# Optimization experiments

Measured on AMD Instinct MI355X. Metric: run time of the kernel, lower is better.

The kernel has to match this reference:

```python
import jax, jax.numpy as jnp
import numpy as np

N_USERS = 1_000_000
N_ITEMS = 100_000
LATENT = 64
BATCH = 4096


def setup_inputs() -> dict:
    key = jax.random.key(0)
    k1, k2, k3, k4 = jax.random.split(key, 4)
    # Xavier-normal init: std = sqrt(2 / (fan_in + fan_out))
    uw_std = float(np.sqrt(2.0 / (N_USERS + LATENT)))
    iw_std = float(np.sqrt(2.0 / (N_ITEMS + LATENT)))
    return {
        "user_ids": jax.random.randint(k1, (BATCH,), 0, N_USERS, dtype=jnp.int32),
        "item_ids": jax.random.randint(k2, (BATCH,), 0, N_ITEMS, dtype=jnp.int32),
        "user_weight": jax.random.normal(k3, (N_USERS, LATENT), dtype=jnp.float32) * uw_std,
        "item_weight": jax.random.normal(k4, (N_ITEMS, LATENT), dtype=jnp.float32) * iw_std,
        "user_bias": jnp.zeros((N_USERS, 1), dtype=jnp.float32),
        "item_bias": jnp.zeros((N_ITEMS, 1), dtype=jnp.float32),
        "bias": jnp.zeros((1,), dtype=jnp.float32),
    }


def reference(user_ids, item_ids, user_weight, item_weight, user_bias, item_bias, bias):
    # Gather rows for the requested users/items.
    uw = user_weight[user_ids]          # [Bu, d]
    ub = user_bias[user_ids]            # [Bu, 1]
    iw = item_weight[item_ids]          # [Bi, d]
    ib = item_bias[item_ids]            # [Bi, 1]
    # rating[u, i] = <uw_u, iw_i> + ub_u + ib_i + bias
    rating = jnp.einsum("ud,id->ui", uw, iw) + ub + ib.T + bias
    # pass_through_sigmoid=False, so no sigmoid applied.
    return rating
```

## Files before the change

### kernel.cpp

```cpp
#include <hip/hip_runtime.h>


#define BATCH 4096
#define D     64
#define TILE  64

__global__ __launch_bounds__(256) void pmf_tile_kernel(
    const int*   __restrict__ user_ids,
    const int*   __restrict__ item_ids,
    const float* __restrict__ user_weight,
    const float* __restrict__ item_weight,
    const float* __restrict__ user_bias,
    const float* __restrict__ item_bias,
    const float* __restrict__ bias,
    float*       __restrict__ out)
{
    __shared__ float Ut[D][TILE];
    __shared__ float It[D][TILE];
    __shared__ float ubs[TILE];
    __shared__ float ibs[TILE];

    const int t  = threadIdx.x;
    const int bx = blockIdx.x;
    const int by = blockIdx.y;

    const int r = t >> 2;
    const int q = t & 3;
    const int urow = user_ids[by * TILE + r];
    const int irow = item_ids[bx * TILE + r];
    const float* up = user_weight + (size_t)urow * D;
    const float* ip = item_weight + (size_t)irow * D;
    #pragma unroll
    for (int i = 0; i < 4; ++i) {
        const int k0 = q * 4 + i * 16;
        const float4 uv = *(const float4*)(up + k0);
        const float4 iv = *(const float4*)(ip + k0);
        Ut[k0 + 0][r] = uv.x; Ut[k0 + 1][r] = uv.y;
        Ut[k0 + 2][r] = uv.z; Ut[k0 + 3][r] = uv.w;
        It[k0 + 0][r] = iv.x; It[k0 + 1][r] = iv.y;
        It[k0 + 2][r] = iv.z; It[k0 + 3][r] = iv.w;
    }
    if (t < TILE) {
        ubs[t] = user_bias[user_ids[by * TILE + t]];
    } else if (t < 2 * TILE) {
        const int tt = t - TILE;
        ibs[tt] = item_bias[item_ids[bx * TILE + tt]];
    }
    __syncthreads();

    const int tx = t & 15;
    const int ty = t >> 4;

    float acc[4][4] = {{0.f}};
    #pragma unroll 16
    for (int k = 0; k < D; ++k) {
        const float4 u  = *(const float4*)&Ut[k][ty * 4];
        const float4 iv = *(const float4*)&It[k][tx * 4];
        const float uu[4] = {u.x, u.y, u.z, u.w};
        const float ii[4] = {iv.x, iv.y, iv.z, iv.w};
        #pragma unroll
        for (int a = 0; a < 4; ++a)
            #pragma unroll
            for (int b = 0; b < 4; ++b)
                acc[a][b] = fmaf(uu[a], ii[b], acc[a][b]);
    }

    const float gb = bias[0];
    #pragma unroll
    for (int a = 0; a < 4; ++a) {
        const int row = by * TILE + ty * 4 + a;
        const float ub = ubs[ty * 4 + a] + gb;
        float4 o;
        o.x = acc[a][0] + ub + ibs[tx * 4 + 0];
        o.y = acc[a][1] + ub + ibs[tx * 4 + 1];
        o.z = acc[a][2] + ub + ibs[tx * 4 + 2];
        o.w = acc[a][3] + ub + ibs[tx * 4 + 3];
        *(float4*)(out + (size_t)row * BATCH + bx * TILE + tx * 4) = o;
    }
}

extern "C" void kernel_launch(void* const* d_in, const int* in_sizes, int n_in,
                              void* d_out, int out_size, void* d_ws, size_t ws_size,
                              hipStream_t stream) {
    const int*   user_ids    = (const int*)  d_in[0];
    const int*   item_ids    = (const int*)  d_in[1];
    const float* user_weight = (const float*)d_in[2];
    const float* item_weight = (const float*)d_in[3];
    const float* user_bias   = (const float*)d_in[4];
    const float* item_bias   = (const float*)d_in[5];
    const float* bias        = (const float*)d_in[6];
    float* out = (float*)d_out;

    dim3 grid(BATCH / TILE, BATCH / TILE);
    dim3 block(256);
    pmf_tile_kernel<<<grid, block, 0, stream>>>(
        user_ids, item_ids, user_weight, item_weight,
        user_bias, item_bias, bias, out);
}
```

Before: 349.7 us.

## Use bf16 MFMA with 128x128 tiles for the gathered rating outer product

Gathered user and item rows are converted to bf16 in shared memory and the dot products run on 16x16x32 bf16 MFMA instructions instead of scalar FP32 FMAs. Tiles grow from 64x64 to 128x128 with four waves each covering 64x64, and shared rows are padded to reduce bank conflicts. This targets compute throughput, but the kernel writes a 64 MB output and is likely store-bound. The output stores are now scalar and strided per lane rather than float4, and bf16 inputs reduce dot-product precision.

```diff
diff --git a/kernel.cpp b/kernel.cpp
--- a/kernel.cpp
+++ b/kernel.cpp
@@ -3,9 +3,20 @@
 
 #define BATCH 4096
 #define D     64
-#define TILE  64
+#define BM    128
+#define BN    128
+#define ROWSZ 72
 
-__global__ __launch_bounds__(256) void pmf_tile_kernel(
+typedef __attribute__((ext_vector_type(8))) short bf16x8;
+typedef __attribute__((ext_vector_type(4))) float f32x4;
+
+static __device__ __forceinline__ unsigned short f2bf(float x) {
+    unsigned int u = __builtin_bit_cast(unsigned int, x);
+    u += 0x7FFFu + ((u >> 16) & 1u);
+    return (unsigned short)(u >> 16);
+}
+
+__global__ __launch_bounds__(256) void pmf_mfma_kernel(
     const int*   __restrict__ user_ids,
     const int*   __restrict__ item_ids,
     const float* __restrict__ user_weight,
@@ -15,67 +26,88 @@
     const float* __restrict__ bias,
     float*       __restrict__ out)
 {
-    __shared__ float Ut[D][TILE];
-    __shared__ float It[D][TILE];
-    __shared__ float ubs[TILE];
-    __shared__ float ibs[TILE];
+    __shared__ __align__(16) unsigned short Ul[BM * ROWSZ];
+    __shared__ __align__(16) unsigned short Il[BN * ROWSZ];
+    __shared__ float ubs[BM];
+    __shared__ float ibs[BN];
 
     const int t  = threadIdx.x;
     const int bx = blockIdx.x;
     const int by = blockIdx.y;
 
-    const int r = t >> 2;
-    const int q = t & 3;
-    const int urow = user_ids[by * TILE + r];
-    const int irow = item_ids[bx * TILE + r];
-    const float* up = user_weight + (size_t)urow * D;
-    const float* ip = item_weight + (size_t)irow * D;
-    #pragma unroll
-    for (int i = 0; i < 4; ++i) {
-        const int k0 = q * 4 + i * 16;
-        const float4 uv = *(const float4*)(up + k0);
-        const float4 iv = *(const float4*)(ip + k0);
-        Ut[k0 + 0][r] = uv.x; Ut[k0 + 1][r] = uv.y;
-        Ut[k0 + 2][r] = uv.z; Ut[k0 + 3][r] = uv.w;
-        It[k0 + 0][r] = iv.x; It[k0 + 1][r] = iv.y;
-        It[k0 + 2][r] = iv.z; It[k0 + 3][r] = iv.w;
-    }
-    if (t < TILE) {
-        ubs[t] = user_bias[user_ids[by * TILE + t]];
-    } else if (t < 2 * TILE) {
-        const int tt = t - TILE;
-        ibs[tt] = item_bias[item_ids[bx * TILE + tt]];
+    {
+        const int  r   = t & 127;
+        const bool isU = (t < 128);
+        const int  gid = isU ? user_ids[by * BM + r] : item_ids[bx * BN + r];
+        const float* src = (isU ? user_weight : item_weight) + (size_t)gid * D;
+        unsigned short* dst = (isU ? Ul : Il) + r * ROWSZ;
+        #pragma unroll
+        for (int c = 0; c < D; c += 8) {
+            const float4 a = *(const float4*)(src + c);
+            const float4 b = *(const float4*)(src + c + 4);
+            union { bf16x8 v; unsigned short u[8]; } pk;
+            pk.u[0] = f2bf(a.x); pk.u[1] = f2bf(a.y);
+            pk.u[2] = f2bf(a.z); pk.u[3] = f2bf(a.w);
+            pk.u[4] = f2bf(b.x); pk.u[5] = f2bf(b.y);
+            pk.u[6] = f2bf(b.z); pk.u[7] = f2bf(b.w);
+            *(bf16x8*)(dst + c) = pk.v;
+        }
+        const float bv = isU ? user_bias[gid] : item_bias[gid];
+        (isU ? ubs : ibs)[r] = bv;
     }
     __syncthreads();
 
-    const int tx = t & 15;
-    const int ty = t >> 4;
+    const int w    = t >> 6;
+    const int lane = t & 63;
+    const int lo   = lane & 15;
+    const int hi   = lane >> 4;
+    const int wr   = w >> 1;
+    const int wc   = w & 1;
 
-    float acc[4][4] = {{0.f}};
-    #pragma unroll 16
-    for (int k = 0; k < D; ++k) {
-        const float4 u  = *(const float4*)&Ut[k][ty * 4];
-        const float4 iv = *(const float4*)&It[k][tx * 4];
-        const float uu[4] = {u.x, u.y, u.z, u.w};
-        const float ii[4] = {iv.x, iv.y, iv.z, iv.w};
+    f32x4 acc[4][4];
+    #pragma unroll
+    for (int m = 0; m < 4; ++m)
         #pragma unroll
-        for (int a = 0; a < 4; ++a)
+        for (int n = 0; n < 4; ++n)
+            acc[m][n] = (f32x4){0.f, 0.f, 0.f, 0.f};
+
+    #pragma unroll
+    for (int kh = 0; kh < 2; ++kh) {
+        const int koff = kh * 32 + hi * 8;
+        bf16x8 af[4], bf[4];
+        #pragma unroll
+        for (int m = 0; m < 4; ++m)
+            af[m] = *(const bf16x8*)&Ul[(wr * 64 + m * 16 + lo) * ROWSZ + koff];
+        #pragma unroll
+        for (int n = 0; n < 4; ++n)
+            bf[n] = *(const bf16x8*)&Il[(wc * 64 + n * 16 + lo) * ROWSZ + koff];
+        #pragma unroll
+        for (int m = 0; m < 4; ++m)
             #pragma unroll
-            for (int b = 0; b < 4; ++b)
-                acc[a][b] = fmaf(uu[a], ii[b], acc[a][b]);
+            for (int n = 0; n < 4; ++n)
+                acc[m][n] = __builtin_amdgcn_mfma_f32_16x16x32_bf16(
+                    af[m], bf[n], acc[m][n], 0, 0, 0);
     }
 
     const float gb = bias[0];
+    float ib4[4];
     #pragma unroll
-    for (int a = 0; a < 4; ++a) {
-        const int row = by * TILE + ty * 4 + a;
-        const float ub = ubs[ty * 4 + a] + gb;
-        float4 o;
-        o.x = acc[a][0] + ub + ibs[tx * 4 + 0];
-        o.y = acc[a][1] + ub + ibs[tx * 4 + 1];
-        o.z = acc[a][2] + ub + ibs[tx * 4 + 2];
-        o.w = acc[a][3] + ub + ibs[tx * 4 + 3];
-        *(float4*)(out + (size_t)row * BATCH + bx * TILE + tx * 4) = o;
+    for (int n = 0; n < 4; ++n) ib4[n] = ibs[wc * 64 + n * 16 + lo];
+
+    const int orow0 = by * BM + wr * 64 + hi * 4;
+    const int ocol0 = bx * BN + wc * 64 + lo;
+    float* op = out + (size_t)orow0 * BATCH + ocol0;
+
+    #pragma unroll
+    for (int m = 0; m < 4; ++m) {
+        #pragma unroll
+        for (int r = 0; r < 4; ++r) {
+            const float ub = ubs[wr * 64 + m * 16 + hi * 4 + r] + gb;
+            const size_t rowoff = (size_t)(m * 16 + r) * BATCH;
+            #pragma unroll
+            for (int n = 0; n < 4; ++n)
+                op[rowoff + n * 16] = acc[m][n][r] + ub + ib4[n];
+        }
     }
 }
 
@@ -91,9 +123,9 @@
     const float* bias        = (const float*)d_in[6];
     float* out = (float*)d_out;
 
-    dim3 grid(BATCH / TILE, BATCH / TILE);
+    dim3 grid(BATCH / BN, BATCH / BM);
     dim3 block(256);
-    pmf_tile_kernel<<<grid, block, 0, stream>>>(
+    pmf_mfma_kernel<<<grid, block, 0, stream>>>(
         user_ids, item_ids, user_weight, item_weight,
         user_bias, item_bias, bias, out);
 }
```

After: 334.1 us. -4.5%, faster.
